# Optimization experiments

Hardware: AMD Instinct MI355X
Metric: run time of the kernel (lower is better)

The kernel has to match this reference:

```python
import jax, jax.numpy as jnp
import numpy as np

B, C, T, V, H = 64, 256, 64, 25, 512


def setup_inputs() -> dict:
    key = jax.random.key(0)
    k_h, k_w1, k_w2, k_r = jax.random.split(key, 4)
    h = jax.random.normal(k_h, (B, C, T, V), dtype=jnp.float32)
    W1 = jax.random.normal(k_w1, (C, H), dtype=jnp.float32) * 0.02
    b1 = jnp.zeros((H,), dtype=jnp.float32)
    W2 = jax.random.normal(k_w2, (H, C), dtype=jnp.float32) * 0.02
    b2 = jnp.zeros((C,), dtype=jnp.float32)
    # per-step teacher-forcing uniforms, one per (timestep, batch elem)
    tf_rand = jax.random.uniform(k_r, (T - 1, B), dtype=jnp.float32)
    return {"h": h, "W1": W1, "b1": b1, "W2": W2, "b2": b2,
            "tf_rand": tf_rand, "t_obs": 16}


def reference(h, W1, b1, W2, b2, tf_rand, t_obs):
    # training=True, run_backwards=False branch of ODEEulerSolver.forward
    # ode_func: 2-layer MLP over the channel dim (time index unused)
    def ode(z):  # z: [B, C, V]
        u = jnp.tanh(jnp.einsum('bcv,ch->bhv', z, W1) + b1[None, :, None])
        return jnp.einsum('bhv,hc->bcv', u, W2) + b2[None, :, None]

    z0 = h[:, :, 0, :]                           # [B, C, V]
    h_prev = jnp.moveaxis(h[:, :, :-1, :], 2, 0)  # [T-1, B, C, V] teacher states

    def step(z_prev, inp):
        h_t, r = inp                              # h_t: [B,C,V], r: [B]
        # rand < 0.5 -> keep previous prediction, else teacher-force h[:, :, t-1]
        mask = (r < 0.5)[:, None, None]
        z_t = jnp.where(mask, z_prev, h_t)
        z_next = z_t + ode(z_t)                   # Euler step
        return z_next, z_next

    _, zs = jax.lax.scan(step, z0, (h_prev, tf_rand))  # zs: [T-1, B, C, V]
    z_hat = jnp.concatenate([z0[:, :, None, :], jnp.moveaxis(zs, 0, 2)], axis=2)
    return z_hat  # [B, C, T, V]
```

## Files before the change

kernel.cpp:

```cpp
#include <hip/hip_runtime.h>
#include <hip/hip_bf16.h>
#include <math.h>


using bf16x8 = __attribute__((ext_vector_type(8))) short;
using f32x4  = __attribute__((ext_vector_type(4))) float;

constexpr int Bb = 64, Cc = 256, Tt = 64, Vv = 25, Hh = 512;
constexpr int TV = Tt * Vv;
constexpr int NCOL = 128;
constexpr int NT = NCOL / 16;
constexpr int MAXCH = Bb * (Tt - 1);
constexpr int NGRID = 2496;

__device__ __forceinline__ short f2bf(float x) {
  union { float f; unsigned u; } v; v.f = x;
  unsigned r = v.u + 0x7FFFu + ((v.u >> 16) & 1u);
  return (short)(r >> 16);
}
__device__ __forceinline__ float fast_tanh(float x) {
  float e = __expf(2.f * x);
  return 1.f - 2.f * __builtin_amdgcn_rcpf(e + 1.f);
}

__global__ void prep_kernel(const float* __restrict__ W1,
                            const float* __restrict__ W2,
                            const float* __restrict__ tf,
                            short* __restrict__ a1p,
                            short* __restrict__ a2p,
                            int* __restrict__ sorted,
                            int* __restrict__ hdr) {
  if (blockIdx.x < 1024) {
    int idx = blockIdx.x * 256 + threadIdx.x;
    if (idx < 131072) {
      int j = idx & 7, lane = (idx >> 3) & 63, mt = (idx >> 9) & 31, kt = idx >> 14;
      int h = mt * 16 + (lane & 15);
      int c = kt * 32 + (lane >> 4) * 8 + j;
      a1p[idx] = f2bf(W1[c * Hh + h]);
    } else {
      int i2 = idx - 131072;
      int j = i2 & 7, lane = (i2 >> 3) & 63, mt = (i2 >> 9) & 15, kt = i2 >> 13;
      int cm = mt * 16 + (lane & 15);
      int hk = kt * 32 + (lane >> 4) * 8 + j;
      a2p[i2] = f2bf(W2[hk * Cc + cm]);
    }
    return;
  }
  __shared__ int cnt[64];
  __shared__ int ofs[64];
  int tid = threadIdx.x;
  if (tid < 64) cnt[tid] = 0;
  for (int i = tid; i < MAXCH; i += 256) sorted[i] = 0;
  __syncthreads();
  if (tid < Bb) {
    int b = tid, prev = 0;
    for (int t = 1; t <= 62; t++)
      if (tf[t * Bb + b] >= 0.5f) { atomicAdd(&cnt[t - prev], 1); prev = t; }
    atomicAdd(&cnt[63 - prev], 1);
  }
  __syncthreads();
  if (tid == 0) {
    int acc = 0;
    for (int l = 63; l >= 1; l--) { ofs[l] = acc; acc += cnt[l]; }
    int n1 = 0;
    for (int l = 5; l <= 63; l++) n1 += cnt[l];
    int n2 = cnt[3] + cnt[4];
    int nch = acc;
    int g2 = (n2 + 1) >> 1;
    int q0 = n1 + 2 * g2;
    int rem = nch - q0; if (rem < 0) rem = 0;
    int g4 = (rem + 3) >> 2;
    hdr[0] = n1; hdr[1] = g2; hdr[2] = g4; hdr[3] = q0;
  }
  __syncthreads();
  if (tid < Bb) {
    int b = tid, prev = 0;
    for (int t = 1; t <= 62; t++) {
      if (tf[t * Bb + b] >= 0.5f) {
        int len = t - prev;
        int p = atomicAdd(&ofs[len], 1);
        sorted[p] = b | (prev << 6) | (len << 12);
        prev = t;
      }
    }
    int len = 63 - prev;
    int p = atomicAdd(&ofs[len], 1);
    sorted[p] = b | (prev << 6) | (len << 12);
  }
}

__global__ __launch_bounds__(512, 2) void group_kernel(
    const float* __restrict__ hsrc, const float* __restrict__ b1,
    const float* __restrict__ b2,   const short* __restrict__ a1p,
    const short* __restrict__ a2p,  const int* __restrict__ sorted,
    const int* __restrict__ hdr,    float* __restrict__ out) {
  __shared__ __align__(16) short zB[8 * NT * 64 * 8];
  __shared__ __align__(16) short uB[8 * NT * 64 * 8];
  __shared__ int s_meta[4];

  const int n1 = hdr[0], g2 = hdr[1], g4 = hdr[2], q0 = hdr[3];
  const int bi = blockIdx.x;
  int start, gsz;
  if (bi < n1)                { start = bi;                        gsz = 1; }
  else if (bi < n1 + g2)      { start = n1 + (bi - n1) * 2;        gsz = 2; }
  else if (bi < n1 + g2 + g4) { start = q0 + (bi - n1 - g2) * 4;   gsz = 4; }
  else return;

  const int tid = threadIdx.x;
  if (tid < 4) s_meta[tid] = (tid < gsz) ? sorted[start + tid] : 0;
  __syncthreads();
  const int maxlen = (s_meta[0] >> 12) & 63;
  const int ntMax  = gsz * 2;

  const int lane = tid & 63;
  const int w    = tid >> 6;
  const int m16  = lane & 15;
  const int quad = lane >> 4;

  int len4[4];
  #pragma unroll
  for (int j = 0; j < 4; j++) len4[j] = (s_meta[j] >> 12) & 63;

  f32x4 acc2[2][NT];
  int   obase[2][NT];

  #pragma unroll
  for (int i = 0; i < 2; i++) {
    const int cbase = (w * 2 + i) * 16 + quad * 4;
    const int ktz = cbase >> 5;
    const int gq  = (cbase >> 3) & 3;
    const int j0  = cbase & 7;
    #pragma unroll
    for (int nt = 0; nt < NT; nt++) {
      if (nt >= ntMax) break;
      const int j  = nt >> 1;
      const int mj = s_meta[j];
      const int bj = mj & 63, t0 = (mj >> 6) & 63;
      const int v  = (nt & 1) * 16 + m16;
      const bool valid = (len4[j] > 0) && (v < Vv);
      const int hb = ((bj * Cc + cbase) * Tt + t0) * Vv + v;
      f32x4 z;
      #pragma unroll
      for (int r = 0; r < 4; r++) z[r] = valid ? hsrc[hb + r * TV] : 0.f;
      acc2[i][nt] = z;
      obase[i][nt] = hb;
      short4 zh;
      zh.x = f2bf(z[0]); zh.y = f2bf(z[1]); zh.z = f2bf(z[2]); zh.w = f2bf(z[3]);
      *(short4*)&zB[((ktz * NT + nt) * 64 + m16 + 16 * gq) * 8 + j0] = zh;
      if (valid && t0 == 0) {
        #pragma unroll
        for (int r = 0; r < 4; r++) out[hb + r * TV] = z[r];
      }
    }
  }
  __syncthreads();

  for (int s = 0; s < maxlen; s++) {
    #pragma unroll
    for (int i = 0; i < 2; i++) {
      const int cbase = (w * 2 + i) * 16 + quad * 4;
      const float4 bv = *(const float4*)(b2 + cbase);
      #pragma unroll
      for (int nt = 0; nt < NT; nt++) {
        if (nt >= ntMax) break;
        acc2[i][nt][0] += bv.x; acc2[i][nt][1] += bv.y;
        acc2[i][nt][2] += bv.z; acc2[i][nt][3] += bv.w;
      }
    }
    #pragma unroll
    for (int chunk = 0; chunk < 2; chunk++) {
      f32x4 acc1[2][NT];
      #pragma unroll
      for (int i = 0; i < 2; i++)
        #pragma unroll
        for (int nt = 0; nt < NT; nt++) acc1[i][nt] = (f32x4){0.f, 0.f, 0.f, 0.f};
      #pragma unroll 2
      for (int kt = 0; kt < 8; kt++) {
        const short* ab = a1p + ((kt * 32 + chunk * 16 + w * 2) * 64 + lane) * 8;
        bf16x8 af0 = *(const bf16x8*)ab;
        bf16x8 af1 = *(const bf16x8*)(ab + 512);
        #pragma unroll
        for (int nt = 0; nt < NT; nt++) {
          if (nt >= ntMax) break;
          bf16x8 bz = *(const bf16x8*)&zB[((kt * NT + nt) * 64 + lane) * 8];
          acc1[0][nt] = __builtin_amdgcn_mfma_f32_16x16x32_bf16(af0, bz, acc1[0][nt], 0, 0, 0);
          acc1[1][nt] = __builtin_amdgcn_mfma_f32_16x16x32_bf16(af1, bz, acc1[1][nt], 0, 0, 0);
        }
      }
      __syncthreads();
      #pragma unroll
      for (int i = 0; i < 2; i++) {
        const int mtl   = w * 2 + i;
        const int hl    = mtl * 16 + quad * 4;
        const int hglob = chunk * 256 + hl;
        const int ktl = hl >> 5;
        const int gq  = (hl >> 3) & 3;
        const int j0  = hl & 7;
        const float4 b1v = *(const float4*)(b1 + hglob);
        #pragma unroll
        for (int nt = 0; nt < NT; nt++) {
          if (nt >= ntMax) break;
          short4 up;
          up.x = f2bf(fast_tanh(acc1[i][nt][0] + b1v.x));
          up.y = f2bf(fast_tanh(acc1[i][nt][1] + b1v.y));
          up.z = f2bf(fast_tanh(acc1[i][nt][2] + b1v.z));
          up.w = f2bf(fast_tanh(acc1[i][nt][3] + b1v.w));
          *(short4*)&uB[((ktl * NT + nt) * 64 + m16 + 16 * gq) * 8 + j0] = up;
        }
      }
      __syncthreads();
      #pragma unroll 2
      for (int ktl = 0; ktl < 8; ktl++) {
        const short* ab = a2p + (((chunk * 8 + ktl) * 16 + w * 2) * 64 + lane) * 8;
        bf16x8 af0 = *(const bf16x8*)ab;
        bf16x8 af1 = *(const bf16x8*)(ab + 512);
        #pragma unroll
        for (int nt = 0; nt < NT; nt++) {
          if (nt >= ntMax) break;
          bf16x8 bu = *(const bf16x8*)&uB[((ktl * NT + nt) * 64 + lane) * 8];
          acc2[0][nt] = __builtin_amdgcn_mfma_f32_16x16x32_bf16(af0, bu, acc2[0][nt], 0, 0, 0);
          acc2[1][nt] = __builtin_amdgcn_mfma_f32_16x16x32_bf16(af1, bu, acc2[1][nt], 0, 0, 0);
        }
      }
    }
    #pragma unroll
    for (int i = 0; i < 2; i++) {
      const int cbase = (w * 2 + i) * 16 + quad * 4;
      const int ktz = cbase >> 5;
      const int gq  = (cbase >> 3) & 3;
      const int j0  = cbase & 7;
      #pragma unroll
      for (int nt = 0; nt < NT; nt++) {
        if (nt >= ntMax) break;
        short4 zh;
        zh.x = f2bf(acc2[i][nt][0]); zh.y = f2bf(acc2[i][nt][1]);
        zh.z = f2bf(acc2[i][nt][2]); zh.w = f2bf(acc2[i][nt][3]);
        *(short4*)&zB[((ktz * NT + nt) * 64 + m16 + 16 * gq) * 8 + j0] = zh;
        const int v = (nt & 1) * 16 + m16;
        if (v < Vv && s < len4[nt >> 1]) {
          const int o = obase[i][nt] + (s + 1) * Vv;
          out[o]          = acc2[i][nt][0];
          out[o + TV]     = acc2[i][nt][1];
          out[o + 2 * TV] = acc2[i][nt][2];
          out[o + 3 * TV] = acc2[i][nt][3];
        }
      }
    }
    __syncthreads();
  }
}

extern "C" void kernel_launch(void* const* d_in, const int* in_sizes, int n_in,
                              void* d_out, int out_size, void* d_ws, size_t ws_size,
                              hipStream_t stream) {
  const float* h_ptr = (const float*)d_in[0];
  const float* W1    = (const float*)d_in[1];
  const float* b1    = (const float*)d_in[2];
  const float* W2    = (const float*)d_in[3];
  const float* b2    = (const float*)d_in[4];
  const float* tf    = (const float*)d_in[5];
  float* out = (float*)d_out;

  short* a1p  = (short*)d_ws;
  short* a2p  = a1p + 131072;
  int* sorted = (int*)(a2p + 131072);
  int* hdr    = sorted + MAXCH;

  prep_kernel<<<1025, 256, 0, stream>>>(W1, W2, tf, a1p, a2p, sorted, hdr);
  group_kernel<<<NGRID, 512, 0, stream>>>(h_ptr, b1, b2, a1p, a2p, sorted, hdr, out);
}
```

Baseline: 367.0 us.

## Halve block to 256 threads, 4 M-tiles per wave, drop 4-chain groups

```diff
diff --git a/kernel.cpp b/kernel.cpp
--- a/kernel.cpp
+++ b/kernel.cpp
@@ -8,10 +8,9 @@
 
 constexpr int Bb = 64, Cc = 256, Tt = 64, Vv = 25, Hh = 512;
 constexpr int TV = Tt * Vv;
-constexpr int NCOL = 128;
-constexpr int NT = NCOL / 16;
+constexpr int NT = 4;
 constexpr int MAXCH = Bb * (Tt - 1);
-constexpr int NGRID = 2496;
+constexpr int NGRID = 2080;
 
 __device__ __forceinline__ short f2bf(float x) {
   union { float f; unsigned u; } v; v.f = x;
@@ -64,13 +63,10 @@
     for (int l = 63; l >= 1; l--) { ofs[l] = acc; acc += cnt[l]; }
     int n1 = 0;
     for (int l = 5; l <= 63; l++) n1 += cnt[l];
-    int n2 = cnt[3] + cnt[4];
-    int nch = acc;
-    int g2 = (n2 + 1) >> 1;
-    int q0 = n1 + 2 * g2;
-    int rem = nch - q0; if (rem < 0) rem = 0;
-    int g4 = (rem + 3) >> 2;
-    hdr[0] = n1; hdr[1] = g2; hdr[2] = g4; hdr[3] = q0;
+    hdr[0] = n1;
+    hdr[1] = (acc - n1 + 1) >> 1;
+    hdr[2] = acc;
+    hdr[3] = 0;
   }
   __syncthreads();
   if (tid < Bb) {
@@ -89,25 +85,24 @@
   }
 }
 
-__global__ __launch_bounds__(512, 2) void group_kernel(
+__global__ __launch_bounds__(256, 2) void group_kernel(
     const float* __restrict__ hsrc, const float* __restrict__ b1,
     const float* __restrict__ b2,   const short* __restrict__ a1p,
     const short* __restrict__ a2p,  const int* __restrict__ sorted,
     const int* __restrict__ hdr,    float* __restrict__ out) {
   __shared__ __align__(16) short zB[8 * NT * 64 * 8];
   __shared__ __align__(16) short uB[8 * NT * 64 * 8];
-  __shared__ int s_meta[4];
-
-  const int n1 = hdr[0], g2 = hdr[1], g4 = hdr[2], q0 = hdr[3];
+  __shared__ int s_meta[2];
+
+  const int n1 = hdr[0], npair = hdr[1];
   const int bi = blockIdx.x;
   int start, gsz;
-  if (bi < n1)                { start = bi;                        gsz = 1; }
-  else if (bi < n1 + g2)      { start = n1 + (bi - n1) * 2;        gsz = 2; }
-  else if (bi < n1 + g2 + g4) { start = q0 + (bi - n1 - g2) * 4;   gsz = 4; }
+  if (bi < n1)              { start = bi;                 gsz = 1; }
+  else if (bi < n1 + npair) { start = n1 + (bi - n1) * 2; gsz = 2; }
   else return;
 
   const int tid = threadIdx.x;
-  if (tid < 4) s_meta[tid] = (tid < gsz) ? sorted[start + tid] : 0;
+  if (tid < 2) s_meta[tid] = (tid < gsz) ? sorted[start + tid] : 0;
   __syncthreads();
   const int maxlen = (s_meta[0] >> 12) & 63;
   const int ntMax  = gsz * 2;
@@ -117,16 +112,17 @@
   const int m16  = lane & 15;
   const int quad = lane >> 4;
 
-  int len4[4];
+  int len2[2];
   #pragma unroll
-  for (int j = 0; j < 4; j++) len4[j] = (s_meta[j] >> 12) & 63;
-
-  f32x4 acc2[2][NT];
-  int   obase[2][NT];
+  for (int j = 0; j < 2; j++) len2[j] = (s_meta[j] >> 12) & 63;
+
+  f32x4 acc2[4][NT];
+  f32x4 acc1[4][NT];
+  int   obase[4][NT];
 
   #pragma unroll
-  for (int i = 0; i < 2; i++) {
-    const int cbase = (w * 2 + i) * 16 + quad * 4;
+  for (int i = 0; i < 4; i++) {
+    const int cbase = (w * 4 + i) * 16 + quad * 4;
     const int ktz = cbase >> 5;
     const int gq  = (cbase >> 3) & 3;
     const int j0  = cbase & 7;
@@ -137,7 +133,7 @@
       const int mj = s_meta[j];
       const int bj = mj & 63, t0 = (mj >> 6) & 63;
       const int v  = (nt & 1) * 16 + m16;
-      const bool valid = (len4[j] > 0) && (v < Vv);
+      const bool valid = (len2[j] > 0) && (v < Vv);
       const int hb = ((bj * Cc + cbase) * Tt + t0) * Vv + v;
       f32x4 z;
       #pragma unroll
@@ -155,10 +151,72 @@
   }
   __syncthreads();
 
+  auto MM1 = [&](int chunk) {
+    #pragma unroll
+    for (int i = 0; i < 4; i++)
+      #pragma unroll
+      for (int nt = 0; nt < NT; nt++) acc1[i][nt] = (f32x4){0.f, 0.f, 0.f, 0.f};
+    #pragma unroll 2
+    for (int kt = 0; kt < 8; kt++) {
+      const short* ab = a1p + ((kt * 32 + chunk * 16 + w * 4) * 64 + lane) * 8;
+      bf16x8 af[4];
+      #pragma unroll
+      for (int i = 0; i < 4; i++) af[i] = *(const bf16x8*)(ab + i * 512);
+      #pragma unroll
+      for (int nt = 0; nt < NT; nt++) {
+        if (nt >= ntMax) break;
+        bf16x8 bz = *(const bf16x8*)&zB[((kt * NT + nt) * 64 + lane) * 8];
+        #pragma unroll
+        for (int i = 0; i < 4; i++)
+          acc1[i][nt] = __builtin_amdgcn_mfma_f32_16x16x32_bf16(af[i], bz, acc1[i][nt], 0, 0, 0);
+      }
+    }
+  };
+
+  auto UEPI = [&](int chunk) {
+    #pragma unroll
+    for (int i = 0; i < 4; i++) {
+      const int hl    = (w * 4 + i) * 16 + quad * 4;
+      const int hglob = chunk * 256 + hl;
+      const int ktl = hl >> 5;
+      const int gq  = (hl >> 3) & 3;
+      const int j0  = hl & 7;
+      const float4 b1v = *(const float4*)(b1 + hglob);
+      #pragma unroll
+      for (int nt = 0; nt < NT; nt++) {
+        if (nt >= ntMax) break;
+        short4 up;
+        up.x = f2bf(fast_tanh(acc1[i][nt][0] + b1v.x));
+        up.y = f2bf(fast_tanh(acc1[i][nt][1] + b1v.y));
+        up.z = f2bf(fast_tanh(acc1[i][nt][2] + b1v.z));
+        up.w = f2bf(fast_tanh(acc1[i][nt][3] + b1v.w));
+        *(short4*)&uB[((ktl * NT + nt) * 64 + m16 + 16 * gq) * 8 + j0] = up;
+      }
+    }
+  };
+
+  auto MM2 = [&](int chunk) {
+    #pragma unroll 2
+    for (int ktl = 0; ktl < 8; ktl++) {
+      const short* ab = a2p + (((chunk * 8 + ktl) * 16 + w * 4) * 64 + lane) * 8;
+      bf16x8 af[4];
+      #pragma unroll
+      for (int i = 0; i < 4; i++) af[i] = *(const bf16x8*)(ab + i * 512);
+      #pragma unroll
+      for (int nt = 0; nt < NT; nt++) {
+        if (nt >= ntMax) break;
+        bf16x8 bu = *(const bf16x8*)&uB[((ktl * NT + nt) * 64 + lane) * 8];
+        #pragma unroll
+        for (int i = 0; i < 4; i++)
+          acc2[i][nt] = __builtin_amdgcn_mfma_f32_16x16x32_bf16(af[i], bu, acc2[i][nt], 0, 0, 0);
+      }
+    }
+  };
+
   for (int s = 0; s < maxlen; s++) {
     #pragma unroll
-    for (int i = 0; i < 2; i++) {
-      const int cbase = (w * 2 + i) * 16 + quad * 4;
+    for (int i = 0; i < 4; i++) {
+      const int cbase = (w * 4 + i) * 16 + quad * 4;
       const float4 bv = *(const float4*)(b2 + cbase);
       #pragma unroll
       for (int nt = 0; nt < NT; nt++) {
@@ -167,65 +225,18 @@
         acc2[i][nt][2] += bv.z; acc2[i][nt][3] += bv.w;
       }
     }
-    #pragma unroll
-    for (int chunk = 0; chunk < 2; chunk++) {
-      f32x4 acc1[2][NT];
-      #pragma unroll
-      for (int i = 0; i < 2; i++)
-        #pragma unroll
-        for (int nt = 0; nt < NT; nt++) acc1[i][nt] = (f32x4){0.f, 0.f, 0.f, 0.f};
-      #pragma unroll 2
-      for (int kt = 0; kt < 8; kt++) {
-        const short* ab = a1p + ((kt * 32 + chunk * 16 + w * 2) * 64 + lane) * 8;
-        bf16x8 af0 = *(const bf16x8*)ab;
-        bf16x8 af1 = *(const bf16x8*)(ab + 512);
-        #pragma unroll
-        for (int nt = 0; nt < NT; nt++) {
-          if (nt >= ntMax) break;
-          bf16x8 bz = *(const bf16x8*)&zB[((kt * NT + nt) * 64 + lane) * 8];
-          acc1[0][nt] = __builtin_amdgcn_mfma_f32_16x16x32_bf16(af0, bz, acc1[0][nt], 0, 0, 0);
-          acc1[1][nt] = __builtin_amdgcn_mfma_f32_16x16x32_bf16(af1, bz, acc1[1][nt], 0, 0, 0);
-        }
-      }
-      __syncthreads();
-      #pragma unroll
-      for (int i = 0; i < 2; i++) {
-        const int mtl   = w * 2 + i;
-        const int hl    = mtl * 16 + quad * 4;
-        const int hglob = chunk * 256 + hl;
-        const int ktl = hl >> 5;
-        const int gq  = (hl >> 3) & 3;
-        const int j0  = hl & 7;
-        const float4 b1v = *(const float4*)(b1 + hglob);
-        #pragma unroll
-        for (int nt = 0; nt < NT; nt++) {
-          if (nt >= ntMax) break;
-          short4 up;
-          up.x = f2bf(fast_tanh(acc1[i][nt][0] + b1v.x));
-          up.y = f2bf(fast_tanh(acc1[i][nt][1] + b1v.y));
-          up.z = f2bf(fast_tanh(acc1[i][nt][2] + b1v.z));
-          up.w = f2bf(fast_tanh(acc1[i][nt][3] + b1v.w));
-          *(short4*)&uB[((ktl * NT + nt) * 64 + m16 + 16 * gq) * 8 + j0] = up;
-        }
-      }
-      __syncthreads();
-      #pragma unroll 2
-      for (int ktl = 0; ktl < 8; ktl++) {
-        const short* ab = a2p + (((chunk * 8 + ktl) * 16 + w * 2) * 64 + lane) * 8;
-        bf16x8 af0 = *(const bf16x8*)ab;
-        bf16x8 af1 = *(const bf16x8*)(ab + 512);
-        #pragma unroll
-        for (int nt = 0; nt < NT; nt++) {
-          if (nt >= ntMax) break;
-          bf16x8 bu = *(const bf16x8*)&uB[((ktl * NT + nt) * 64 + lane) * 8];
-          acc2[0][nt] = __builtin_amdgcn_mfma_f32_16x16x32_bf16(af0, bu, acc2[0][nt], 0, 0, 0);
-          acc2[1][nt] = __builtin_amdgcn_mfma_f32_16x16x32_bf16(af1, bu, acc2[1][nt], 0, 0, 0);
-        }
-      }
-    }
-    #pragma unroll
-    for (int i = 0; i < 2; i++) {
-      const int cbase = (w * 2 + i) * 16 + quad * 4;
+    MM1(0);
+    UEPI(0);
+    __syncthreads();
+    MM2(0);
+    MM1(1);
+    __syncthreads();
+    UEPI(1);
+    __syncthreads();
+    MM2(1);
+    #pragma unroll
+    for (int i = 0; i < 4; i++) {
+      const int cbase = (w * 4 + i) * 16 + quad * 4;
       const int ktz = cbase >> 5;
       const int gq  = (cbase >> 3) & 3;
       const int j0  = cbase & 7;
@@ -237,7 +248,7 @@
         zh.z = f2bf(acc2[i][nt][2]); zh.w = f2bf(acc2[i][nt][3]);
         *(short4*)&zB[((ktz * NT + nt) * 64 + m16 + 16 * gq) * 8 + j0] = zh;
         const int v = (nt & 1) * 16 + m16;
-        if (v < Vv && s < len4[nt >> 1]) {
+        if (v < Vv && s < len2[nt >> 1]) {
           const int o = obase[i][nt] + (s + 1) * Vv;
           out[o]          = acc2[i][nt][0];
           out[o + TV]     = acc2[i][nt][1];
@@ -267,5 +278,5 @@
   int* hdr    = sorted + MAXCH;
 
   prep_kernel<<<1025, 256, 0, stream>>>(W1, W2, tf, a1p, a2p, sorted, hdr);
-  group_kernel<<<NGRID, 512, 0, stream>>>(h_ptr, b1, b2, a1p, a2p, sorted, hdr, out);
-}
+  group_kernel<<<NGRID, 256, 0, stream>>>(h_ptr, b1, b2, a1p, a2p, sorted, hdr, out);
+}
```

Measured after the change: 380.7 us. +3.7%, slower.
